# Kernel tuning notes

Hardware: AMD Instinct MI355X
Metric: run time of the kernel (lower is better)

The kernel has to match this reference:

```python
import jax, jax.numpy as jnp
import numpy as np

H, W = 4096, 4096
KH, KW = 16, 16


def setup_inputs() -> dict:
    key = jax.random.key(0)
    kx, kw = jax.random.split(key)
    x = jax.random.normal(kx, (H, W), dtype=jnp.float32)
    weight = jax.random.normal(kw, (KH, KW), dtype=jnp.float32)
    bias = jnp.zeros((1,), dtype=jnp.float32)
    return {"x": x, "weight": weight, "bias": bias}


def reference(x, weight, bias):
    # 2D valid cross-correlation (no kernel flip), single channel, + scalar bias.
    # lax.conv_general_dilated computes cross-correlation by default.
    lhs = x[None, None, :, :]          # [1,1,H,W]
    rhs = weight[None, None, :, :]     # [1,1,KH,KW]
    y = jax.lax.conv_general_dilated(
        lhs, rhs,
        window_strides=(1, 1),
        padding="VALID",
        dimension_numbers=("NCHW", "OIHW", "NCHW"),
    )[0, 0]                            # [H-KH+1, W-KW+1]
    return y + bias[0]
```

## Files before the change

### kernel.cpp

```cpp
#include <hip/hip_runtime.h>

#define IH 4096
#define IW 4096
#define KH 16
#define KW 16
#define OH 4081
#define OW 4081

#define TBR 64
#define TBC 128
#define LROWS 79
#define LSTR 192

typedef short bf16x8 __attribute__((ext_vector_type(8)));
typedef float f32x4  __attribute__((ext_vector_type(4)));

static __device__ __forceinline__ unsigned int f2bf(float f) {
    unsigned int u = __float_as_uint(f);
    return (u + 0x7FFFu + ((u >> 16) & 1u)) >> 16;
}

__global__ void build_B(const float* __restrict__ wgt, unsigned short* __restrict__ Btab) {
    int idx = blockIdx.x * 256 + threadIdx.x;
    if (idx >= 16 * 16 * 32) return;
    int vp = idx & 31;
    int n  = (idx >> 5) & 15;
    int u  = idx >> 9;
    int t  = vp - n;
    float val = (t >= 0 && t < KW) ? wgt[u * KW + t] : 0.0f;
    Btab[idx] = (unsigned short)f2bf(val);
}

__global__ __launch_bounds__(512, 8)
void conv_mfma(const float* __restrict__ x,
               const unsigned short* __restrict__ Btab,
               const float* __restrict__ bias,
               float* __restrict__ out) {
    __shared__ unsigned short tile[LROWS * LSTR];

    const int tid  = threadIdx.x;
    const int lane = tid & 63;
    const int wv   = tid >> 6;
    const int n    = lane & 15;
    const int q4   = lane >> 4;
    const int gy0  = blockIdx.y * TBR;
    const int gx0  = blockIdx.x * TBC;

    for (int idx = tid; idx < LROWS * 36; idx += 512) {
        int row = idx / 36;
        int c   = idx - row * 36;
        int gy  = gy0 + row;
        int gx  = gx0 + 4 * c;
        float4 q = make_float4(0.f, 0.f, 0.f, 0.f);
        if (gy < IH) {
            if (gx + 4 <= IW) {
                q = *reinterpret_cast<const float4*>(x + (size_t)gy * IW + gx);
            } else {
                float e0 = (gx + 0 < IW) ? x[(size_t)gy * IW + gx + 0] : 0.f;
                float e1 = (gx + 1 < IW) ? x[(size_t)gy * IW + gx + 1] : 0.f;
                float e2 = (gx + 2 < IW) ? x[(size_t)gy * IW + gx + 2] : 0.f;
                float e3 = (gx + 3 < IW) ? x[(size_t)gy * IW + gx + 3] : 0.f;
                q = make_float4(e0, e1, e2, e3);
            }
        }
        uint2 packed;
        packed.x = f2bf(q.x) | (f2bf(q.y) << 16);
        packed.y = f2bf(q.z) | (f2bf(q.w) << 16);
        int chunk = c >> 1;
        int half  = c & 1;
        int phys  = chunk ^ (row & 7);
        *reinterpret_cast<uint2*>(&tile[row * LSTR + phys * 8 + half * 4]) = packed;
    }
    __syncthreads();

    const int rb  = wv >> 1;
    const int cg  = wv & 1;
    const int li0 = rb * 16;

    f32x4 acc0 = {0.f, 0.f, 0.f, 0.f};
    f32x4 acc1 = {0.f, 0.f, 0.f, 0.f};
    f32x4 acc2 = {0.f, 0.f, 0.f, 0.f};
    f32x4 acc3 = {0.f, 0.f, 0.f, 0.f};

    const int cbase = cg * 8 + q4;
    const unsigned short* bbase = Btab + n * 32 + q4 * 8;

#pragma unroll
    for (int u = 0; u < KH; ++u) {
        bf16x8 bf = *reinterpret_cast<const bf16x8*>(bbase + u * 512);
        int row = li0 + n + u;
        int swz = row & 7;
        const unsigned short* rbase = &tile[row * LSTR];
        bf16x8 a0 = *reinterpret_cast<const bf16x8*>(rbase + ((cbase + 0) ^ swz) * 8);
        bf16x8 a1 = *reinterpret_cast<const bf16x8*>(rbase + ((cbase + 2) ^ swz) * 8);
        bf16x8 a2 = *reinterpret_cast<const bf16x8*>(rbase + ((cbase + 4) ^ swz) * 8);
        bf16x8 a3 = *reinterpret_cast<const bf16x8*>(rbase + ((cbase + 6) ^ swz) * 8);
        acc0 = __builtin_amdgcn_mfma_f32_16x16x32_bf16(a0, bf, acc0, 0, 0, 0);
        acc1 = __builtin_amdgcn_mfma_f32_16x16x32_bf16(a1, bf, acc1, 0, 0, 0);
        acc2 = __builtin_amdgcn_mfma_f32_16x16x32_bf16(a2, bf, acc2, 0, 0, 0);
        acc3 = __builtin_amdgcn_mfma_f32_16x16x32_bf16(a3, bf, acc3, 0, 0, 0);
    }

    const float bv = bias[0];
    const int orow0 = gy0 + li0 + q4 * 4;
    const int ocol0 = gx0 + cg * 64 + n;

#pragma unroll
    for (int t = 0; t < 4; ++t) {
        const f32x4 acc = (t == 0) ? acc0 : (t == 1) ? acc1 : (t == 2) ? acc2 : acc3;
        int col = ocol0 + t * 16;
        if (col < OW) {
#pragma unroll
            for (int r = 0; r < 4; ++r) {
                int rr = orow0 + r;
                if (rr < OH) out[(size_t)rr * OW + col] = acc[r] + bv;
            }
        }
    }
}

extern "C" void kernel_launch(void* const* d_in, const int* in_sizes, int n_in,
                              void* d_out, int out_size, void* d_ws, size_t ws_size,
                              hipStream_t stream) {
    const float* x  = (const float*)d_in[0];
    const float* w  = (const float*)d_in[1];
    const float* b  = (const float*)d_in[2];
    float* out = (float*)d_out;
    unsigned short* Btab = (unsigned short*)d_ws;

    build_B<<<32, 256, 0, stream>>>(w, Btab);

    dim3 grid((OW + TBC - 1) / TBC, (OH + TBR - 1) / TBR);
    conv_mfma<<<grid, dim3(512), 0, stream>>>(x, Btab, b, out);
}
```

Baseline: 138.7 us.

## Make conv blocks persistent over four column tiles with double-buffered LDS prefetch

Each block now processes four consecutive 128-column tiles. The next tile's global loads are issued into registers before the MFMA loop on the current tile, then converted and written into a second LDS buffer afterwards. The MFMA inner loop also software-pipelines its LDS and B reads one step ahead. The aim is to hide global-load latency behind compute, at the cost of more registers, lower occupancy (launch bounds drop from 8 to 4 blocks) and a grid cut to 512 blocks, which may underfill the GPU.

```diff
diff --git a/kernel.cpp b/kernel.cpp
--- a/kernel.cpp
+++ b/kernel.cpp
@@ -9,8 +9,10 @@
 
 #define TBR 64
 #define TBC 128
+#define NT  4
 #define LROWS 79
 #define LSTR 192
+#define NLOAD (LROWS * 36)
 
 typedef short bf16x8 __attribute__((ext_vector_type(8)));
 typedef float f32x4  __attribute__((ext_vector_type(4)));
@@ -31,12 +33,59 @@
     Btab[idx] = (unsigned short)f2bf(val);
 }
 
-__global__ __launch_bounds__(512, 8)
+static __device__ __forceinline__ void load_tile(const float* __restrict__ x,
+                                                 int gy0, int gx0, int tid,
+                                                 float4 (&g)[6]) {
+#pragma unroll
+    for (int s = 0; s < 6; ++s) {
+        int idx = tid + s * 512;
+        float4 q = make_float4(0.f, 0.f, 0.f, 0.f);
+        if (s < 5 || tid < (NLOAD - 5 * 512)) {
+            int row = idx / 36;
+            int c   = idx - row * 36;
+            int gy  = gy0 + row;
+            int gx  = gx0 + 4 * c;
+            if (gy < IH) {
+                if (gx + 4 <= IW) {
+                    q = *reinterpret_cast<const float4*>(x + (size_t)gy * IW + gx);
+                } else {
+                    float e0 = (gx + 0 < IW) ? x[(size_t)gy * IW + gx + 0] : 0.f;
+                    float e1 = (gx + 1 < IW) ? x[(size_t)gy * IW + gx + 1] : 0.f;
+                    float e2 = (gx + 2 < IW) ? x[(size_t)gy * IW + gx + 2] : 0.f;
+                    float e3 = (gx + 3 < IW) ? x[(size_t)gy * IW + gx + 3] : 0.f;
+                    q = make_float4(e0, e1, e2, e3);
+                }
+            }
+        }
+        g[s] = q;
+    }
+}
+
+static __device__ __forceinline__ void cvt_write(const float4 (&g)[6],
+                                                 unsigned short* buf, int tid) {
+#pragma unroll
+    for (int s = 0; s < 6; ++s) {
+        int idx = tid + s * 512;
+        if (s < 5 || tid < (NLOAD - 5 * 512)) {
+            int row = idx / 36;
+            int c   = idx - row * 36;
+            uint2 packed;
+            packed.x = f2bf(g[s].x) | (f2bf(g[s].y) << 16);
+            packed.y = f2bf(g[s].z) | (f2bf(g[s].w) << 16);
+            int chunk = c >> 1;
+            int half  = c & 1;
+            int phys  = chunk ^ (row & 7);
+            *reinterpret_cast<uint2*>(&buf[row * LSTR + phys * 8 + half * 4]) = packed;
+        }
+    }
+}
+
+__global__ __launch_bounds__(512, 4)
 void conv_mfma(const float* __restrict__ x,
                const unsigned short* __restrict__ Btab,
                const float* __restrict__ bias,
                float* __restrict__ out) {
-    __shared__ unsigned short tile[LROWS * LSTR];
+    __shared__ unsigned short tile[2][LROWS * LSTR];
 
     const int tid  = threadIdx.x;
     const int lane = tid & 63;
@@ -44,77 +93,89 @@
     const int n    = lane & 15;
     const int q4   = lane >> 4;
     const int gy0  = blockIdx.y * TBR;
-    const int gx0  = blockIdx.x * TBC;
-
-    for (int idx = tid; idx < LROWS * 36; idx += 512) {
-        int row = idx / 36;
-        int c   = idx - row * 36;
-        int gy  = gy0 + row;
-        int gx  = gx0 + 4 * c;
-        float4 q = make_float4(0.f, 0.f, 0.f, 0.f);
-        if (gy < IH) {
-            if (gx + 4 <= IW) {
-                q = *reinterpret_cast<const float4*>(x + (size_t)gy * IW + gx);
-            } else {
-                float e0 = (gx + 0 < IW) ? x[(size_t)gy * IW + gx + 0] : 0.f;
-                float e1 = (gx + 1 < IW) ? x[(size_t)gy * IW + gx + 1] : 0.f;
-                float e2 = (gx + 2 < IW) ? x[(size_t)gy * IW + gx + 2] : 0.f;
-                float e3 = (gx + 3 < IW) ? x[(size_t)gy * IW + gx + 3] : 0.f;
-                q = make_float4(e0, e1, e2, e3);
-            }
-        }
-        uint2 packed;
-        packed.x = f2bf(q.x) | (f2bf(q.y) << 16);
-        packed.y = f2bf(q.z) | (f2bf(q.w) << 16);
-        int chunk = c >> 1;
-        int half  = c & 1;
-        int phys  = chunk ^ (row & 7);
-        *reinterpret_cast<uint2*>(&tile[row * LSTR + phys * 8 + half * 4]) = packed;
-    }
-    __syncthreads();
+    const int gx_base = blockIdx.x * (NT * TBC);
 
     const int rb  = wv >> 1;
     const int cg  = wv & 1;
     const int li0 = rb * 16;
-
-    f32x4 acc0 = {0.f, 0.f, 0.f, 0.f};
-    f32x4 acc1 = {0.f, 0.f, 0.f, 0.f};
-    f32x4 acc2 = {0.f, 0.f, 0.f, 0.f};
-    f32x4 acc3 = {0.f, 0.f, 0.f, 0.f};
-
     const int cbase = cg * 8 + q4;
     const unsigned short* bbase = Btab + n * 32 + q4 * 8;
+    const float bv = bias[0];
+
+    {
+        float4 g0[6];
+        load_tile(x, gy0, gx_base, tid, g0);
+        cvt_write(g0, &tile[0][0], tid);
+    }
+    __syncthreads();
+
+#pragma unroll 1
+    for (int j = 0; j < NT; ++j) {
+        const int gx0 = gx_base + j * TBC;
+        const bool pre = (j + 1 < NT);
+
+        float4 gn[6];
+        if (pre) load_tile(x, gy0, gx0 + TBC, tid, gn);
+
+        const unsigned short* buf = &tile[j & 1][0];
+
+        f32x4 acc0 = {0.f, 0.f, 0.f, 0.f};
+        f32x4 acc1 = {0.f, 0.f, 0.f, 0.f};
+        f32x4 acc2 = {0.f, 0.f, 0.f, 0.f};
+        f32x4 acc3 = {0.f, 0.f, 0.f, 0.f};
+
+        bf16x8 b_c = *reinterpret_cast<const bf16x8*>(bbase);
+        {
+        }
+        int row0 = li0 + n;
+        int swz0 = row0 & 7;
+        const unsigned short* rb0 = buf + row0 * LSTR;
+        bf16x8 a_c0 = *reinterpret_cast<const bf16x8*>(rb0 + ((cbase + 0) ^ swz0) * 8);
+        bf16x8 a_c1 = *reinterpret_cast<const bf16x8*>(rb0 + ((cbase + 2) ^ swz0) * 8);
+        bf16x8 a_c2 = *reinterpret_cast<const bf16x8*>(rb0 + ((cbase + 4) ^ swz0) * 8);
+        bf16x8 a_c3 = *reinterpret_cast<const bf16x8*>(rb0 + ((cbase + 6) ^ swz0) * 8);
 
 #pragma unroll
-    for (int u = 0; u < KH; ++u) {
-        bf16x8 bf = *reinterpret_cast<const bf16x8*>(bbase + u * 512);
-        int row = li0 + n + u;
-        int swz = row & 7;
-        const unsigned short* rbase = &tile[row * LSTR];
-        bf16x8 a0 = *reinterpret_cast<const bf16x8*>(rbase + ((cbase + 0) ^ swz) * 8);
-        bf16x8 a1 = *reinterpret_cast<const bf16x8*>(rbase + ((cbase + 2) ^ swz) * 8);
-        bf16x8 a2 = *reinterpret_cast<const bf16x8*>(rbase + ((cbase + 4) ^ swz) * 8);
-        bf16x8 a3 = *reinterpret_cast<const bf16x8*>(rbase + ((cbase + 6) ^ swz) * 8);
-        acc0 = __builtin_amdgcn_mfma_f32_16x16x32_bf16(a0, bf, acc0, 0, 0, 0);
-        acc1 = __builtin_amdgcn_mfma_f32_16x16x32_bf16(a1, bf, acc1, 0, 0, 0);
-        acc2 = __builtin_amdgcn_mfma_f32_16x16x32_bf16(a2, bf, acc2, 0, 0, 0);
-        acc3 = __builtin_amdgcn_mfma_f32_16x16x32_bf16(a3, bf, acc3, 0, 0, 0);
-    }
+        for (int u = 0; u < KH; ++u) {
+            bf16x8 b_n, a_n0, a_n1, a_n2, a_n3;
+            if (u < KH - 1) {
+                b_n = *reinterpret_cast<const bf16x8*>(bbase + (u + 1) * 512);
+                int row = li0 + n + u + 1;
+                int swz = row & 7;
+                const unsigned short* rbn = buf + row * LSTR;
+                a_n0 = *reinterpret_cast<const bf16x8*>(rbn + ((cbase + 0) ^ swz) * 8);
+                a_n1 = *reinterpret_cast<const bf16x8*>(rbn + ((cbase + 2) ^ swz) * 8);
+                a_n2 = *reinterpret_cast<const bf16x8*>(rbn + ((cbase + 4) ^ swz) * 8);
+                a_n3 = *reinterpret_cast<const bf16x8*>(rbn + ((cbase + 6) ^ swz) * 8);
+            }
+            acc0 = __builtin_amdgcn_mfma_f32_16x16x32_bf16(a_c0, b_c, acc0, 0, 0, 0);
+            acc1 = __builtin_amdgcn_mfma_f32_16x16x32_bf16(a_c1, b_c, acc1, 0, 0, 0);
+            acc2 = __builtin_amdgcn_mfma_f32_16x16x32_bf16(a_c2, b_c, acc2, 0, 0, 0);
+            acc3 = __builtin_amdgcn_mfma_f32_16x16x32_bf16(a_c3, b_c, acc3, 0, 0, 0);
+            if (u < KH - 1) {
+                b_c = b_n;
+                a_c0 = a_n0; a_c1 = a_n1; a_c2 = a_n2; a_c3 = a_n3;
+            }
+        }
 
-    const float bv = bias[0];
-    const int orow0 = gy0 + li0 + q4 * 4;
-    const int ocol0 = gx0 + cg * 64 + n;
+        const int orow0 = gy0 + li0 + q4 * 4;
+        const int ocol0 = gx0 + cg * 64 + n;
+#pragma unroll
+        for (int t = 0; t < 4; ++t) {
+            const f32x4 acc = (t == 0) ? acc0 : (t == 1) ? acc1 : (t == 2) ? acc2 : acc3;
+            int col = ocol0 + t * 16;
+            if (col < OW) {
+#pragma unroll
+                for (int r = 0; r < 4; ++r) {
+                    int rr = orow0 + r;
+                    if (rr < OH) out[(size_t)rr * OW + col] = acc[r] + bv;
+                }
+            }
+        }
 
-#pragma unroll
-    for (int t = 0; t < 4; ++t) {
-        const f32x4 acc = (t == 0) ? acc0 : (t == 1) ? acc1 : (t == 2) ? acc2 : acc3;
-        int col = ocol0 + t * 16;
-        if (col < OW) {
-#pragma unroll
-            for (int r = 0; r < 4; ++r) {
-                int rr = orow0 + r;
-                if (rr < OH) out[(size_t)rr * OW + col] = acc[r] + bv;
-            }
+        if (pre) {
+            cvt_write(gn, &tile[(j + 1) & 1][0], tid);
+            __syncthreads();
         }
     }
 }
@@ -130,6 +191,6 @@
 
     build_B<<<32, 256, 0, stream>>>(w, Btab);
 
-    dim3 grid((OW + TBC - 1) / TBC, (OH + TBR - 1) / TBR);
+    dim3 grid(8, 64);
     conv_mfma<<<grid, dim3(512), 0, stream>>>(x, Btab, b, out);
 }
```

Result: slower. 325.0 us (+134.3%).

## Process four column tiles per block with async LDS prefetch of next tile

Applied to the files above, without the earlier changes.

Each block now walks four adjacent 128-column output tiles instead of one. While MFMAs run on the current tile, it issues global_load_lds transfers of the next tile's fp32 input into a raw LDS staging buffer, then converts that buffer to the swizzled bf16 tile after a barrier. Edge handling changes from branchy zero-fill loads to clamped addresses, and the grid shrinks to 8x64 blocks. The intent is to hide global load latency behind compute, at the cost of a large extra LDS buffer that lowers blocks per CU, a serial per-block loop, and a dependence on barriers waiting for the async loads to finish.

```diff
diff --git a/kernel.cpp b/kernel.cpp
--- a/kernel.cpp
+++ b/kernel.cpp
@@ -9,8 +9,11 @@
 
 #define TBR 64
 #define TBC 128
+#define NT  4
 #define LROWS 79
 #define LSTR 192
+#define NLOAD (LROWS * 36)
+#define RSLOTS (6 * 512)
 
 typedef short bf16x8 __attribute__((ext_vector_type(8)));
 typedef float f32x4  __attribute__((ext_vector_type(4)));
@@ -31,12 +34,13 @@
     Btab[idx] = (unsigned short)f2bf(val);
 }
 
-__global__ __launch_bounds__(512, 8)
+__global__ __launch_bounds__(512, 4)
 void conv_mfma(const float* __restrict__ x,
                const unsigned short* __restrict__ Btab,
                const float* __restrict__ bias,
                float* __restrict__ out) {
     __shared__ unsigned short tile[LROWS * LSTR];
+    __shared__ float4 raw[RSLOTS];
 
     const int tid  = threadIdx.x;
     const int lane = tid & 63;
@@ -44,25 +48,23 @@
     const int n    = lane & 15;
     const int q4   = lane >> 4;
     const int gy0  = blockIdx.y * TBR;
-    const int gx0  = blockIdx.x * TBC;
+    const int gx_base = blockIdx.x * (NT * TBC);
 
-    for (int idx = tid; idx < LROWS * 36; idx += 512) {
+    const int rb  = wv >> 1;
+    const int cg  = wv & 1;
+    const int li0 = rb * 16;
+    const int cbase = cg * 8 + q4;
+    const unsigned short* bbase = Btab + n * 32 + q4 * 8;
+    const float bv = bias[0];
+
+    for (int idx = tid; idx < NLOAD; idx += 512) {
         int row = idx / 36;
         int c   = idx - row * 36;
         int gy  = gy0 + row;
-        int gx  = gx0 + 4 * c;
-        float4 q = make_float4(0.f, 0.f, 0.f, 0.f);
-        if (gy < IH) {
-            if (gx + 4 <= IW) {
-                q = *reinterpret_cast<const float4*>(x + (size_t)gy * IW + gx);
-            } else {
-                float e0 = (gx + 0 < IW) ? x[(size_t)gy * IW + gx + 0] : 0.f;
-                float e1 = (gx + 1 < IW) ? x[(size_t)gy * IW + gx + 1] : 0.f;
-                float e2 = (gx + 2 < IW) ? x[(size_t)gy * IW + gx + 2] : 0.f;
-                float e3 = (gx + 3 < IW) ? x[(size_t)gy * IW + gx + 3] : 0.f;
-                q = make_float4(e0, e1, e2, e3);
-            }
-        }
+        int gx  = gx_base + 4 * c;
+        int cy  = gy < IH ? gy : IH - 1;
+        int cx  = gx <= IW - 4 ? gx : IW - 4;
+        float4 q = *reinterpret_cast<const float4*>(x + (size_t)cy * IW + cx);
         uint2 packed;
         packed.x = f2bf(q.x) | (f2bf(q.y) << 16);
         packed.y = f2bf(q.z) | (f2bf(q.w) << 16);
@@ -73,48 +75,82 @@
     }
     __syncthreads();
 
-    const int rb  = wv >> 1;
-    const int cg  = wv & 1;
-    const int li0 = rb * 16;
+#pragma unroll 1
+    for (int j = 0; j < NT; ++j) {
+        const int gx0 = gx_base + j * TBC;
+        const bool pre = (j + 1 < NT);
 
-    f32x4 acc0 = {0.f, 0.f, 0.f, 0.f};
-    f32x4 acc1 = {0.f, 0.f, 0.f, 0.f};
-    f32x4 acc2 = {0.f, 0.f, 0.f, 0.f};
-    f32x4 acc3 = {0.f, 0.f, 0.f, 0.f};
+        if (pre) {
+            const int gxn = gx0 + TBC;
+#pragma unroll
+            for (int s = 0; s < 6; ++s) {
+                int idx = s * 512 + tid;
+                int row = idx / 36;
+                int c   = idx - row * 36;
+                int gy  = gy0 + row;
+                int gx  = gxn + 4 * c;
+                int cy  = gy < IH ? gy : IH - 1;
+                int cx  = gx <= IW - 4 ? gx : IW - 4;
+                const float* gp = x + (size_t)cy * IW + cx;
+                __builtin_amdgcn_global_load_lds(
+                    (const __attribute__((address_space(1))) void*)gp,
+                    (__attribute__((address_space(3))) void*)&raw[s * 512 + wv * 64],
+                    16, 0, 0);
+            }
+        }
 
-    const int cbase = cg * 8 + q4;
-    const unsigned short* bbase = Btab + n * 32 + q4 * 8;
+        f32x4 acc0 = {0.f, 0.f, 0.f, 0.f};
+        f32x4 acc1 = {0.f, 0.f, 0.f, 0.f};
+        f32x4 acc2 = {0.f, 0.f, 0.f, 0.f};
+        f32x4 acc3 = {0.f, 0.f, 0.f, 0.f};
 
 #pragma unroll
-    for (int u = 0; u < KH; ++u) {
-        bf16x8 bf = *reinterpret_cast<const bf16x8*>(bbase + u * 512);
-        int row = li0 + n + u;
-        int swz = row & 7;
-        const unsigned short* rbase = &tile[row * LSTR];
-        bf16x8 a0 = *reinterpret_cast<const bf16x8*>(rbase + ((cbase + 0) ^ swz) * 8);
-        bf16x8 a1 = *reinterpret_cast<const bf16x8*>(rbase + ((cbase + 2) ^ swz) * 8);
-        bf16x8 a2 = *reinterpret_cast<const bf16x8*>(rbase + ((cbase + 4) ^ swz) * 8);
-        bf16x8 a3 = *reinterpret_cast<const bf16x8*>(rbase + ((cbase + 6) ^ swz) * 8);
-        acc0 = __builtin_amdgcn_mfma_f32_16x16x32_bf16(a0, bf, acc0, 0, 0, 0);
-        acc1 = __builtin_amdgcn_mfma_f32_16x16x32_bf16(a1, bf, acc1, 0, 0, 0);
-        acc2 = __builtin_amdgcn_mfma_f32_16x16x32_bf16(a2, bf, acc2, 0, 0, 0);
-        acc3 = __builtin_amdgcn_mfma_f32_16x16x32_bf16(a3, bf, acc3, 0, 0, 0);
-    }
+        for (int u = 0; u < KH; ++u) {
+            bf16x8 bf = *reinterpret_cast<const bf16x8*>(bbase + u * 512);
+            int row = li0 + n + u;
+            int swz = row & 7;
+            const unsigned short* rbase = &tile[row * LSTR];
+            bf16x8 a0 = *reinterpret_cast<const bf16x8*>(rbase + ((cbase + 0) ^ swz) * 8);
+            bf16x8 a1 = *reinterpret_cast<const bf16x8*>(rbase + ((cbase + 2) ^ swz) * 8);
+            bf16x8 a2 = *reinterpret_cast<const bf16x8*>(rbase + ((cbase + 4) ^ swz) * 8);
+            bf16x8 a3 = *reinterpret_cast<const bf16x8*>(rbase + ((cbase + 6) ^ swz) * 8);
+            acc0 = __builtin_amdgcn_mfma_f32_16x16x32_bf16(a0, bf, acc0, 0, 0, 0);
+            acc1 = __builtin_amdgcn_mfma_f32_16x16x32_bf16(a1, bf, acc1, 0, 0, 0);
+            acc2 = __builtin_amdgcn_mfma_f32_16x16x32_bf16(a2, bf, acc2, 0, 0, 0);
+            acc3 = __builtin_amdgcn_mfma_f32_16x16x32_bf16(a3, bf, acc3, 0, 0, 0);
+        }
 
-    const float bv = bias[0];
-    const int orow0 = gy0 + li0 + q4 * 4;
-    const int ocol0 = gx0 + cg * 64 + n;
+        const int orow0 = gy0 + li0 + q4 * 4;
+        const int ocol0 = gx0 + cg * 64 + n;
+#pragma unroll
+        for (int t = 0; t < 4; ++t) {
+            const f32x4 acc = (t == 0) ? acc0 : (t == 1) ? acc1 : (t == 2) ? acc2 : acc3;
+            int col = ocol0 + t * 16;
+            if (col < OW) {
+#pragma unroll
+                for (int r = 0; r < 4; ++r) {
+                    int rr = orow0 + r;
+                    if (rr < OH) out[(size_t)rr * OW + col] = acc[r] + bv;
+                }
+            }
+        }
 
-#pragma unroll
-    for (int t = 0; t < 4; ++t) {
-        const f32x4 acc = (t == 0) ? acc0 : (t == 1) ? acc1 : (t == 2) ? acc2 : acc3;
-        int col = ocol0 + t * 16;
-        if (col < OW) {
-#pragma unroll
-            for (int r = 0; r < 4; ++r) {
-                int rr = orow0 + r;
-                if (rr < OH) out[(size_t)rr * OW + col] = acc[r] + bv;
+        __syncthreads();
+
+        if (pre) {
+            for (int idx = tid; idx < NLOAD; idx += 512) {
+                float4 q = raw[idx];
+                int row = idx / 36;
+                int c   = idx - row * 36;
+                uint2 packed;
+                packed.x = f2bf(q.x) | (f2bf(q.y) << 16);
+                packed.y = f2bf(q.z) | (f2bf(q.w) << 16);
+                int chunk = c >> 1;
+                int half  = c & 1;
+                int phys  = chunk ^ (row & 7);
+                *reinterpret_cast<uint2*>(&tile[row * LSTR + phys * 8 + half * 4]) = packed;
             }
+            __syncthreads();
         }
     }
 }
@@ -130,6 +166,6 @@
 
     build_B<<<32, 256, 0, stream>>>(w, Btab);
 
-    dim3 grid((OW + TBC - 1) / TBC, (OH + TBR - 1) / TBR);
+    dim3 grid(8, 64);
     conv_mfma<<<grid, dim3(512), 0, stream>>>(x, Btab, b, out);
 }
```

Result: slower. 200.7 us (+44.7%).
